# Optimization experiments

Measured on AMD Instinct MI355X. Metric: run time of the kernel, lower is better.

## Reference

```python
import jax, jax.numpy as jnp
import numpy as np

BN_EPS = 1e-5


def setup_inputs() -> dict:
    key = jax.random.key(0)
    ks = jax.random.split(key, 4)
    N, C, T, V, S = 64, 64, 300, 25, 3
    x = jax.random.normal(ks[0], (N, C, T, V), dtype=jnp.float32)
    PA = jax.random.uniform(ks[1], (S, V, V), dtype=jnp.float32)
    # 1x1 conv weights per subset, branch-init scale sqrt(2/(out*1*1*branches))
    Wc = jax.random.normal(ks[2], (S, C, C), dtype=jnp.float32) * np.sqrt(2.0 / (C * S))
    bc = jnp.zeros((S, C), dtype=jnp.float32)
    gamma = jnp.ones((C,), dtype=jnp.float32)
    beta = jnp.zeros((C,), dtype=jnp.float32)
    return {"x": x, "PA": PA, "Wc": Wc, "bc": bc, "gamma": gamma, "beta": beta}


def reference(x, PA, Wc, bc, gamma, beta):
    # x: [N,C,T,V]; PA: [S,V,V]; Wc: [S,Cout,Cin]; bc: [S,Cout]
    # L2_norm: per-column L2 norm along dim=1 of each subset adjacency
    A = PA / (jnp.linalg.norm(PA, axis=1, keepdims=True) + 1e-4)  # [S,V,V]
    # For each subset: (x.view(N,CT,V) @ A[s]) then 1x1 conv, summed over subsets.
    # out[n,o,t,w] = sum_s sum_c sum_v x[n,c,t,v] * A[s,v,w] * Wc[s,o,c] + sum_s bc[s,o]
    y = jnp.einsum('nctv,svw,soc->notw', x, A, Wc)
    y = y + bc.sum(axis=0)[None, :, None, None]
    # BatchNorm2d (training-mode batch statistics) over (N,T,V) per channel
    mean = y.mean(axis=(0, 2, 3), keepdims=True)
    var = y.var(axis=(0, 2, 3), keepdims=True)
    y = (y - mean) * jax.lax.rsqrt(var + BN_EPS)
    y = y * gamma[None, :, None, None] + beta[None, :, None, None]
    # residual (identity since in_channels == out_channels) + ReLU
    return jax.nn.relu(y + x)
```

## Files before the change

kernel.cpp:

```cpp
#include <hip/hip_runtime.h>
#include <hip/hip_bf16.h>
#include <math.h>

typedef __attribute__((ext_vector_type(8))) short short8v;
typedef __attribute__((ext_vector_type(4))) float f32x4;

#define NB 64
#define CC 64
#define TT 300
#define VV 25
#define SS 3
#define TB 4
#define TBLK (TT/TB)

#define AFA_BYTES 36864
#define WCF_BYTES 49152
#define YOFF_BYTES 131072

static __device__ __forceinline__ unsigned short f2bf(float f){
    union { __hip_bfloat16 h; unsigned short s; } u;
    u.h = __float2bfloat16(f);
    return u.s;
}
static __device__ __forceinline__ float bf2f(unsigned short b){
    return __uint_as_float(((unsigned)b) << 16);
}
static __device__ __forceinline__ void pack2(const f32x4& z, unsigned& d0, unsigned& d1){
    d0 = (unsigned)f2bf(z[0]) | ((unsigned)f2bf(z[1]) << 16);
    d1 = (unsigned)f2bf(z[2]) | ((unsigned)f2bf(z[3]) << 16);
}
static __device__ __forceinline__ short8v mk8(unsigned q0,unsigned q1,unsigned q2,unsigned q3){
    union { unsigned u[4]; short8v v; } x;
    x.u[0]=q0; x.u[1]=q1; x.u[2]=q2; x.u[3]=q3;
    return x.v;
}

__global__ void gcn_prep(const float* __restrict__ PA, const float* __restrict__ Wc,
                         float* __restrict__ ws)
{
    __shared__ float inv[SS][VV];
    const int tid = threadIdx.x;
    for (int i = tid; i < 8192; i += 384) ws[i] = 0.f;
    if (tid < SS*VV){
        int s = tid/VV, w = tid%VV;
        float sum = 0.f;
        for (int v=0; v<VV; ++v){ float p = PA[s*VV*VV + v*VV + w]; sum = fmaf(p,p,sum); }
        inv[s][w] = 1.f/(sqrtf(sum)+1e-4f);
    }
    __syncthreads();
    {
        int s = tid/128, rem = tid%128, nt = rem/64, lane = rem%64;
        int w = nt*16 + (lane&15), g = lane>>4;
        short8v vals;
        #pragma unroll
        for (int j=0;j<8;++j){
            int v = 8*g + j;
            float f = (v<VV && w<VV) ? PA[s*VV*VV + v*VV + w]*inv[s][w] : 0.f;
            vals[j] = (short)f2bf(f);
        }
        *(short8v*)((char*)ws + AFA_BYTES + (size_t)((s*2+nt)*64 + lane)*16) = vals;
    }
    for (int fid = tid; fid < SS*4*2*64; fid += 384){
        int lane = fid & 63;
        int kt = (fid >> 6) & 1;
        int ot = (fid >> 7) & 3;
        int s  = fid >> 9;
        int o  = 16*ot + (lane & 15);
        int c0 = kt*32 + 8*(lane >> 4);
        short8v vals;
        #pragma unroll
        for (int j=0;j<8;++j) vals[j] = (short)f2bf(Wc[((size_t)s*CC + o)*CC + c0 + j]);
        *(short8v*)((char*)ws + WCF_BYTES + (size_t)fid*16) = vals;
    }
}

#define XPITCH 36

template<bool YB>
__global__ __launch_bounds__(256,6) void gcn_main_kernel(
    const float* __restrict__ x, float* __restrict__ ws,
    float* __restrict__ yf32, __hip_bfloat16* __restrict__ ybf)
{
    __shared__ __align__(16) unsigned short lds[256*XPITCH];

    const int tid  = threadIdx.x;
    const int lane = tid & 63;
    const int wv   = tid >> 6;
    const int l15  = lane & 15, g = lane >> 4;
    const int n    = blockIdx.x / TBLK;
    const int t0   = (blockIdx.x % TBLK) * TB;

    lds[tid*XPITCH + 25] = 0;
    *(unsigned*)&lds[tid*XPITCH + 26] = 0u;
    *(uint2*)&lds[tid*XPITCH + 28] = make_uint2(0u,0u);

    const float4* x4 = (const float4*)(x + ((size_t)n*CC*TT + t0)*VV);
    for (int i4 = tid; i4 < CC*TB*VV/4; i4 += 256){
        int c = i4 / (TB*VV/4);
        int j = i4 % (TB*VV/4);
        float4 v4 = x4[c*(TT*VV/4) + j];
        float vals[4] = {v4.x, v4.y, v4.z, v4.w};
        int e = 4*j;
        #pragma unroll
        for (int k=0;k<4;++k){
            int ee = e+k;
            lds[((ee/VV)*64 + c)*XPITCH + (ee%VV)] = f2bf(vals[k]);
        }
    }
    __syncthreads();

    short8v axf[4];
    #pragma unroll
    for (int mt=0; mt<4; ++mt){
        const unsigned short* rp = &lds[(wv*64 + 16*mt + l15)*XPITCH + 8*g];
        uint2 lo = *(const uint2*)rp;
        uint2 hi = *(const uint2*)(rp + 4);
        axf[mt] = mk8(lo.x, lo.y, hi.x, hi.y);
    }

    const short8v* afrag = (const short8v*)((const char*)ws + AFA_BYTES);
    const short8v* wfrag = (const short8v*)((const char*)ws + WCF_BYTES);

    const f32x4 zf = {0.f,0.f,0.f,0.f};
    f32x4 yacc[4][2];
    #pragma unroll
    for (int ot=0; ot<4; ++ot){ yacc[ot][0]=zf; yacc[ot][1]=zf; }

    const int sLo = 32*(g&1) + l15;
    const int sHi = sLo + 16;
    const bool hi = (lane >= 32);

    #pragma unroll 1
    for (int s=0; s<SS; ++s){
        short8v aA0 = afrag[(s*2+0)*64 + lane];
        short8v aA1 = afrag[(s*2+1)*64 + lane];
        #pragma unroll
        for (int kt=0; kt<2; ++kt){
            f32x4 z00 = __builtin_amdgcn_mfma_f32_16x16x32_bf16(axf[2*kt+0], aA0, zf, 0,0,0);
            f32x4 z01 = __builtin_amdgcn_mfma_f32_16x16x32_bf16(axf[2*kt+0], aA1, zf, 0,0,0);
            f32x4 z10 = __builtin_amdgcn_mfma_f32_16x16x32_bf16(axf[2*kt+1], aA0, zf, 0,0,0);
            f32x4 z11 = __builtin_amdgcn_mfma_f32_16x16x32_bf16(axf[2*kt+1], aA1, zf, 0,0,0);
            unsigned pLo0n0, pLo1n0, pLo0n1, pLo1n1;
            unsigned pHi0n0, pHi1n0, pHi0n1, pHi1n1;
            pack2(z00, pLo0n0, pLo1n0);
            pack2(z01, pLo0n1, pLo1n1);
            pack2(z10, pHi0n0, pHi1n0);
            pack2(z11, pHi0n1, pHi1n1);
            unsigned a0,b0,a1,b1,a2,b2,a3,b3;
            a0=__shfl(pLo0n0,sLo); b0=__shfl(pHi0n0,sLo);
            a1=__shfl(pLo1n0,sLo); b1=__shfl(pHi1n0,sLo);
            a2=__shfl(pLo0n0,sHi); b2=__shfl(pHi0n0,sHi);
            a3=__shfl(pLo1n0,sHi); b3=__shfl(pHi1n0,sHi);
            short8v bz0 = mk8(hi?b0:a0, hi?b1:a1, hi?b2:a2, hi?b3:a3);
            a0=__shfl(pLo0n1,sLo); b0=__shfl(pHi0n1,sLo);
            a1=__shfl(pLo1n1,sLo); b1=__shfl(pHi1n1,sLo);
            a2=__shfl(pLo0n1,sHi); b2=__shfl(pHi0n1,sHi);
            a3=__shfl(pLo1n1,sHi); b3=__shfl(pHi1n1,sHi);
            short8v bz1 = mk8(hi?b0:a0, hi?b1:a1, hi?b2:a2, hi?b3:a3);
            #pragma unroll
            for (int ot=0; ot<4; ++ot){
                short8v wc = wfrag[((s*4+ot)*2+kt)*64 + lane];
                yacc[ot][0] = __builtin_amdgcn_mfma_f32_16x16x32_bf16(wc, bz0, yacc[ot][0], 0,0,0);
                yacc[ot][1] = __builtin_amdgcn_mfma_f32_16x16x32_bf16(wc, bz1, yacc[ot][1], 0,0,0);
            }
        }
    }

    __syncthreads();
    #pragma unroll
    for (int ot=0; ot<4; ++ot){
        #pragma unroll
        for (int r=0; r<4; ++r){
            const int o = 16*ot + 4*g + r;
            lds[o*100 + wv*25 + l15] = f2bf(yacc[ot][0][r]);
            if (l15 < VV-16)
                lds[o*100 + wv*25 + 16 + l15] = f2bf(yacc[ot][1][r]);
        }
    }
    __syncthreads();

    for (int i = tid; i < 1600; i += 256){
        const int row = i / 25;
        const int c8  = i % 25;
        uint2 d = *(const uint2*)&lds[row*100 + c8*4];
        const size_t base = (size_t)(n*CC + row)*(TT*VV) + (size_t)t0*VV + c8*4;
        if (YB){
            *(uint2*)((unsigned short*)ybf + base) = d;
        } else {
            float4 f;
            f.x = bf2f((unsigned short)(d.x & 0xffff));
            f.y = bf2f((unsigned short)(d.x >> 16));
            f.z = bf2f((unsigned short)(d.y & 0xffff));
            f.w = bf2f((unsigned short)(d.y >> 16));
            *(float4*)(yf32 + base) = f;
        }
    }

    {
        const int o = tid >> 2, q = tid & 3;
        float s1 = 0.f, s2 = 0.f;
        #pragma unroll
        for (int k=0; k<VV; ++k){
            float v = bf2f(lds[o*100 + q*25 + k]);
            s1 += v;
            s2 = fmaf(v, v, s2);
        }
        s1 += __shfl_xor(s1,1); s1 += __shfl_xor(s1,2);
        s2 += __shfl_xor(s2,1); s2 += __shfl_xor(s2,2);
        if (q == 0){
            atomicAdd(&ws[n*128 + o],      s1);
            atomicAdd(&ws[n*128 + 64 + o], s2);
        }
    }
}

__global__ void gcn_finalize_kernel(const float* __restrict__ gamma,
                                    const float* __restrict__ beta,
                                    float* __restrict__ ws)
{
    const int o = threadIdx.x;
    if (o < CC) {
        float s = 0.f, q = 0.f;
        for (int n = 0; n < NB; ++n){
            s += ws[n*128 + o];
            q += ws[n*128 + 64 + o];
        }
        const float cnt = (float)(NB * TT * VV);
        const float mean = s / cnt;
        const float var  = q / cnt - mean * mean;
        const float sc   = gamma[o] * rsqrtf(var + 1e-5f);
        ws[8192 + o] = sc;
        ws[8256 + o] = beta[o] - mean * sc;
    }
}

template<bool YB>
__global__ __launch_bounds__(256) void gcn_bn_relu_kernel(
    const float* __restrict__ x, float* __restrict__ out,
    const float* __restrict__ ws, const unsigned short* __restrict__ ybf)
{
    const int total4 = NB * CC * TT * VV / 4;
    const int per_c4 = TT * VV / 4;
    for (int i = blockIdx.x * 256 + threadIdx.x; i < total4; i += gridDim.x * 256) {
        const int c = (i / per_c4) & (CC - 1);
        const float sc = ws[8192 + c];
        const float sh = ws[8256 + c];
        float4 yv;
        if (YB){
            uint2 yb = *(const uint2*)&ybf[4*i];
            yv.x = bf2f((unsigned short)(yb.x & 0xffff));
            yv.y = bf2f((unsigned short)(yb.x >> 16));
            yv.z = bf2f((unsigned short)(yb.y & 0xffff));
            yv.w = bf2f((unsigned short)(yb.y >> 16));
        } else {
            yv = reinterpret_cast<float4*>(out)[i];
        }
        float4 xv = reinterpret_cast<const float4*>(x)[i];
        float4 r;
        r.x = fmaxf(fmaf(yv.x, sc, sh) + xv.x, 0.f);
        r.y = fmaxf(fmaf(yv.y, sc, sh) + xv.y, 0.f);
        r.z = fmaxf(fmaf(yv.z, sc, sh) + xv.z, 0.f);
        r.w = fmaxf(fmaf(yv.w, sc, sh) + xv.w, 0.f);
        reinterpret_cast<float4*>(out)[i] = r;
    }
}

extern "C" void kernel_launch(void* const* d_in, const int* in_sizes, int n_in,
                              void* d_out, int out_size, void* d_ws, size_t ws_size,
                              hipStream_t stream)
{
    const float* x     = (const float*)d_in[0];
    const float* PA    = (const float*)d_in[1];
    const float* Wc    = (const float*)d_in[2];
    const float* gamma = (const float*)d_in[4];
    const float* beta  = (const float*)d_in[5];
    float* out = (float*)d_out;
    float* ws  = (float*)d_ws;

    const size_t ybytes = (size_t)NB*CC*TT*VV*2;
    const bool yb = ws_size >= (size_t)YOFF_BYTES + ybytes;
    __hip_bfloat16* ybf = (__hip_bfloat16*)((char*)d_ws + YOFF_BYTES);

    gcn_prep<<<1, 384, 0, stream>>>(PA, Wc, ws);
    if (yb){
        gcn_main_kernel<true><<<NB*TBLK, 256, 0, stream>>>(x, ws, out, ybf);
        gcn_finalize_kernel<<<1, 64, 0, stream>>>(gamma, beta, ws);
        gcn_bn_relu_kernel<true><<<2048, 256, 0, stream>>>(x, out, ws, (const unsigned short*)ybf);
    } else {
        gcn_main_kernel<false><<<NB*TBLK, 256, 0, stream>>>(x, ws, out, ybf);
        gcn_finalize_kernel<<<1, 64, 0, stream>>>(gamma, beta, ws);
        gcn_bn_relu_kernel<false><<<2048, 256, 0, stream>>>(x, out, ws, (const unsigned short*)ybf);
    }
}
```

Before: 131.8 us.

## Halve time slab per block and split output channels across wave pairs

Each block now handles two time steps instead of four, and the four waves split work as two slabs by two output-channel halves, each wave accumulating two output tiles instead of four. This cuts per-wave accumulator registers and LDS use, allowing a higher occupancy hint (8 blocks) and twice as many blocks for better load balance. In exchange each wave redoes the first-stage x·A MFMAs for its slab, so that work is duplicated. Global loads and stores narrow from float4/uint2 to float2/uint, and twice as many BN-statistic atomics are issued.

```diff
diff --git a/kernel.cpp b/kernel.cpp
--- a/kernel.cpp
+++ b/kernel.cpp
@@ -10,7 +10,7 @@
 #define TT 300
 #define VV 25
 #define SS 3
-#define TB 4
+#define TB 2
 #define TBLK (TT/TB)
 
 #define AFA_BYTES 36864
@@ -75,44 +75,45 @@
 }
 
 #define XPITCH 36
+#define YPITCH 50
 
 template<bool YB>
-__global__ __launch_bounds__(256,6) void gcn_main_kernel(
+__global__ __launch_bounds__(256,8) void gcn_main_kernel(
     const float* __restrict__ x, float* __restrict__ ws,
     float* __restrict__ yf32, __hip_bfloat16* __restrict__ ybf)
 {
-    __shared__ __align__(16) unsigned short lds[256*XPITCH];
-
-    const int tid  = threadIdx.x;
-    const int lane = tid & 63;
-    const int wv   = tid >> 6;
-    const int l15  = lane & 15, g = lane >> 4;
-    const int n    = blockIdx.x / TBLK;
-    const int t0   = (blockIdx.x % TBLK) * TB;
-
-    lds[tid*XPITCH + 25] = 0;
-    *(unsigned*)&lds[tid*XPITCH + 26] = 0u;
-    *(uint2*)&lds[tid*XPITCH + 28] = make_uint2(0u,0u);
-
-    const float4* x4 = (const float4*)(x + ((size_t)n*CC*TT + t0)*VV);
-    for (int i4 = tid; i4 < CC*TB*VV/4; i4 += 256){
-        int c = i4 / (TB*VV/4);
-        int j = i4 % (TB*VV/4);
-        float4 v4 = x4[c*(TT*VV/4) + j];
-        float vals[4] = {v4.x, v4.y, v4.z, v4.w};
-        int e = 4*j;
-        #pragma unroll
-        for (int k=0;k<4;++k){
-            int ee = e+k;
-            lds[((ee/VV)*64 + c)*XPITCH + (ee%VV)] = f2bf(vals[k]);
-        }
+    __shared__ __align__(16) unsigned short lds[128*XPITCH];
+
+    const int tid   = threadIdx.x;
+    const int lane  = tid & 63;
+    const int wv    = tid >> 6;
+    const int slab  = wv >> 1;
+    const int ohalf = wv & 1;
+    const int l15   = lane & 15, g = lane >> 4;
+    const int n     = blockIdx.x / TBLK;
+    const int t0    = (blockIdx.x % TBLK) * TB;
+
+    if (tid < 128){
+        lds[tid*XPITCH + 25] = 0;
+        *(unsigned*)&lds[tid*XPITCH + 26] = 0u;
+        *(uint2*)&lds[tid*XPITCH + 28] = make_uint2(0u,0u);
+    }
+
+    const float2* x2 = (const float2*)(x + ((size_t)n*CC*TT + t0)*VV);
+    for (int i = tid; i < CC*TB*VV/2; i += 256){
+        int c = i / (TB*VV/2);
+        int j = i % (TB*VV/2);
+        float2 v2 = x2[c*(TT*VV/2) + j];
+        int e0 = 2*j, e1 = 2*j+1;
+        lds[((e0/VV)*CC + c)*XPITCH + (e0%VV)] = f2bf(v2.x);
+        lds[((e1/VV)*CC + c)*XPITCH + (e1%VV)] = f2bf(v2.y);
     }
     __syncthreads();
 
     short8v axf[4];
     #pragma unroll
     for (int mt=0; mt<4; ++mt){
-        const unsigned short* rp = &lds[(wv*64 + 16*mt + l15)*XPITCH + 8*g];
+        const unsigned short* rp = &lds[(slab*CC + 16*mt + l15)*XPITCH + 8*g];
         uint2 lo = *(const uint2*)rp;
         uint2 hi = *(const uint2*)(rp + 4);
         axf[mt] = mk8(lo.x, lo.y, hi.x, hi.y);
@@ -122,9 +123,8 @@
     const short8v* wfrag = (const short8v*)((const char*)ws + WCF_BYTES);
 
     const f32x4 zf = {0.f,0.f,0.f,0.f};
-    f32x4 yacc[4][2];
-    #pragma unroll
-    for (int ot=0; ot<4; ++ot){ yacc[ot][0]=zf; yacc[ot][1]=zf; }
+    f32x4 yacc[2][2];
+    yacc[0][0]=zf; yacc[0][1]=zf; yacc[1][0]=zf; yacc[1][1]=zf;
 
     const int sLo = 32*(g&1) + l15;
     const int sHi = sLo + 16;
@@ -158,55 +158,56 @@
             a3=__shfl(pLo1n1,sHi); b3=__shfl(pHi1n1,sHi);
             short8v bz1 = mk8(hi?b0:a0, hi?b1:a1, hi?b2:a2, hi?b3:a3);
             #pragma unroll
-            for (int ot=0; ot<4; ++ot){
+            for (int i=0; i<2; ++i){
+                const int ot = 2*ohalf + i;
                 short8v wc = wfrag[((s*4+ot)*2+kt)*64 + lane];
-                yacc[ot][0] = __builtin_amdgcn_mfma_f32_16x16x32_bf16(wc, bz0, yacc[ot][0], 0,0,0);
-                yacc[ot][1] = __builtin_amdgcn_mfma_f32_16x16x32_bf16(wc, bz1, yacc[ot][1], 0,0,0);
+                yacc[i][0] = __builtin_amdgcn_mfma_f32_16x16x32_bf16(wc, bz0, yacc[i][0], 0,0,0);
+                yacc[i][1] = __builtin_amdgcn_mfma_f32_16x16x32_bf16(wc, bz1, yacc[i][1], 0,0,0);
             }
         }
     }
 
     __syncthreads();
     #pragma unroll
-    for (int ot=0; ot<4; ++ot){
+    for (int i=0; i<2; ++i){
         #pragma unroll
         for (int r=0; r<4; ++r){
-            const int o = 16*ot + 4*g + r;
-            lds[o*100 + wv*25 + l15] = f2bf(yacc[ot][0][r]);
+            const int o = 16*(2*ohalf + i) + 4*g + r;
+            lds[o*YPITCH + slab*VV + l15] = f2bf(yacc[i][0][r]);
             if (l15 < VV-16)
-                lds[o*100 + wv*25 + 16 + l15] = f2bf(yacc[ot][1][r]);
-        }
-    }
-    __syncthreads();
-
-    for (int i = tid; i < 1600; i += 256){
-        const int row = i / 25;
-        const int c8  = i % 25;
-        uint2 d = *(const uint2*)&lds[row*100 + c8*4];
-        const size_t base = (size_t)(n*CC + row)*(TT*VV) + (size_t)t0*VV + c8*4;
+                lds[o*YPITCH + slab*VV + 16 + l15] = f2bf(yacc[i][1][r]);
+        }
+    }
+    __syncthreads();
+
+    for (int i = tid; i < CC*TB*VV/2; i += 256){
+        const int row = i / (TB*VV/2);
+        const int c2  = i % (TB*VV/2);
+        unsigned d = *(const unsigned*)&lds[row*YPITCH + c2*2];
+        const size_t base = (size_t)(n*CC + row)*(TT*VV) + (size_t)t0*VV + c2*2;
         if (YB){
-            *(uint2*)((unsigned short*)ybf + base) = d;
+            *(unsigned*)((unsigned short*)ybf + base) = d;
         } else {
-            float4 f;
-            f.x = bf2f((unsigned short)(d.x & 0xffff));
-            f.y = bf2f((unsigned short)(d.x >> 16));
-            f.z = bf2f((unsigned short)(d.y & 0xffff));
-            f.w = bf2f((unsigned short)(d.y >> 16));
-            *(float4*)(yf32 + base) = f;
+            float2 f;
+            f.x = bf2f((unsigned short)(d & 0xffff));
+            f.y = bf2f((unsigned short)(d >> 16));
+            *(float2*)(yf32 + base) = f;
         }
     }
 
     {
         const int o = tid >> 2, q = tid & 3;
         float s1 = 0.f, s2 = 0.f;
-        #pragma unroll
-        for (int k=0; k<VV; ++k){
-            float v = bf2f(lds[o*100 + q*25 + k]);
-            s1 += v;
-            s2 = fmaf(v, v, s2);
-        }
-        s1 += __shfl_xor(s1,1); s1 += __shfl_xor(s1,2);
-        s2 += __shfl_xor(s2,1); s2 += __shfl_xor(s2,2);
+        if (q < 2){
+            #pragma unroll
+            for (int k=0; k<VV; ++k){
+                float v = bf2f(lds[o*YPITCH + q*VV + k]);
+                s1 += v;
+                s2 = fmaf(v, v, s2);
+            }
+        }
+        s1 += __shfl_xor(s1,1);
+        s2 += __shfl_xor(s2,1);
         if (q == 0){
             atomicAdd(&ws[n*128 + o],      s1);
             atomicAdd(&ws[n*128 + 64 + o], s2);
```

Result: slower. 182.5 us (+38.5%).

## Load x directly into MFMA fragments from global, dropping the LDS staging

Applied to the files above, without the earlier changes.

Each wave now reads its own time step's x values straight from global memory into bf16 MFMA operand registers. This replaces the cooperative coalesced load, the transpose through LDS and the barrier that followed it. The LDS buffer shrinks to just the output tile, and the launch-bounds occupancy hint rises from 6 to 7. The batch-statistics reduction now reads LDS as packed 4-element chunks. The cost is less coalesced global access: lanes stride across channels, and the float4 loads start at addresses that are not 16-byte aligned.

```diff
diff --git a/kernel.cpp b/kernel.cpp
--- a/kernel.cpp
+++ b/kernel.cpp
@@ -74,14 +74,12 @@
     }
 }
 
-#define XPITCH 36
-
 template<bool YB>
-__global__ __launch_bounds__(256,6) void gcn_main_kernel(
+__global__ __launch_bounds__(256,7) void gcn_main_kernel(
     const float* __restrict__ x, float* __restrict__ ws,
     float* __restrict__ yf32, __hip_bfloat16* __restrict__ ybf)
 {
-    __shared__ __align__(16) unsigned short lds[256*XPITCH];
+    __shared__ __align__(16) unsigned short lds[CC*100];
 
     const int tid  = threadIdx.x;
     const int lane = tid & 63;
@@ -89,33 +87,24 @@
     const int l15  = lane & 15, g = lane >> 4;
     const int n    = blockIdx.x / TBLK;
     const int t0   = (blockIdx.x % TBLK) * TB;
-
-    lds[tid*XPITCH + 25] = 0;
-    *(unsigned*)&lds[tid*XPITCH + 26] = 0u;
-    *(uint2*)&lds[tid*XPITCH + 28] = make_uint2(0u,0u);
-
-    const float4* x4 = (const float4*)(x + ((size_t)n*CC*TT + t0)*VV);
-    for (int i4 = tid; i4 < CC*TB*VV/4; i4 += 256){
-        int c = i4 / (TB*VV/4);
-        int j = i4 % (TB*VV/4);
-        float4 v4 = x4[c*(TT*VV/4) + j];
-        float vals[4] = {v4.x, v4.y, v4.z, v4.w};
-        int e = 4*j;
-        #pragma unroll
-        for (int k=0;k<4;++k){
-            int ee = e+k;
-            lds[((ee/VV)*64 + c)*XPITCH + (ee%VV)] = f2bf(vals[k]);
-        }
-    }
-    __syncthreads();
+    const int t    = t0 + wv;
 
     short8v axf[4];
     #pragma unroll
     for (int mt=0; mt<4; ++mt){
-        const unsigned short* rp = &lds[(wv*64 + 16*mt + l15)*XPITCH + 8*g];
-        uint2 lo = *(const uint2*)rp;
-        uint2 hi = *(const uint2*)(rp + 4);
-        axf[mt] = mk8(lo.x, lo.y, hi.x, hi.y);
+        const int c = 16*mt + l15;
+        const float* p = x + ((size_t)(n*CC + c)*TT + t)*VV + 8*g;
+        short8v f;
+        if (g < 3){
+            float4 a = *(const float4*)p;
+            float4 b = *(const float4*)(p+4);
+            f[0]=(short)f2bf(a.x); f[1]=(short)f2bf(a.y); f[2]=(short)f2bf(a.z); f[3]=(short)f2bf(a.w);
+            f[4]=(short)f2bf(b.x); f[5]=(short)f2bf(b.y); f[6]=(short)f2bf(b.z); f[7]=(short)f2bf(b.w);
+        } else {
+            f[0]=(short)f2bf(p[0]);
+            f[1]=0; f[2]=0; f[3]=0; f[4]=0; f[5]=0; f[6]=0; f[7]=0;
+        }
+        axf[mt] = f;
     }
 
     const short8v* afrag = (const short8v*)((const char*)ws + AFA_BYTES);
@@ -166,7 +155,6 @@
         }
     }
 
-    __syncthreads();
     #pragma unroll
     for (int ot=0; ot<4; ++ot){
         #pragma unroll
@@ -199,11 +187,14 @@
     {
         const int o = tid >> 2, q = tid & 3;
         float s1 = 0.f, s2 = 0.f;
-        #pragma unroll
-        for (int k=0; k<VV; ++k){
-            float v = bf2f(lds[o*100 + q*25 + k]);
-            s1 += v;
-            s2 = fmaf(v, v, s2);
+        for (int gr = q; gr < 25; gr += 4){
+            uint2 d = *(const uint2*)&lds[o*100 + gr*4];
+            float a0 = bf2f((unsigned short)(d.x & 0xffff));
+            float a1 = bf2f((unsigned short)(d.x >> 16));
+            float a2 = bf2f((unsigned short)(d.y & 0xffff));
+            float a3 = bf2f((unsigned short)(d.y >> 16));
+            s1 += (a0+a1)+(a2+a3);
+            s2 = fmaf(a0,a0,fmaf(a1,a1,fmaf(a2,a2,fmaf(a3,a3,s2))));
         }
         s1 += __shfl_xor(s1,1); s1 += __shfl_xor(s1,2);
         s2 += __shfl_xor(s2,1); s2 += __shfl_xor(s2,2);
```

New measurement: 148.3 us. 12.6% more time.
